# Kernel tuning notes

Hardware: AMD Instinct MI355X
Metric: run time of the kernel (lower is better)

## Reference

```python
import jax, jax.numpy as jnp
import numpy as np


def setup_inputs() -> dict:
    key = jax.random.key(0)
    ks = jax.random.split(key, 14)
    n, c, m, s = 32, 256, 32, 64
    rn = lambda k, shape, sc=1.0: jax.random.normal(k, shape, dtype=jnp.float32) * sc
    return {
        "seg_ori": rn(ks[0], (n, c, m, m)),
        "edge_ori": rn(ks[1], (n, c, m, m)),
        "W_s1": rn(ks[2], (s, c), 0.05), "b_s1": rn(ks[3], (s,), 0.05),
        "W_s11": rn(ks[4], (s, c), 0.05), "b_s11": rn(ks[5], (s,), 0.05),
        "W_mlp": rn(ks[6], (s, c), 0.05), "b_mlp": rn(ks[7], (s,), 0.05),
        "w_s2": rn(ks[8], ()), "b_s2": rn(ks[9], ()),
        "w_s3": rn(ks[10], ()), "b_s3": rn(ks[11], ()),
        "W_g": rn(ks[12], (c, c), 0.02), "b_g": rn(ks[13], (c,), 0.02),
    }


def reference(seg_ori, edge_ori, W_s1, b_s1, W_s11, b_s11, W_mlp, b_mlp,
              w_s2, b_s2, w_s3, b_s3, W_g, b_g):
    n, c, m, _ = seg_ori.shape
    hw = m * m                      # num_n = mids^2
    s = W_s1.shape[0]               # num_s = plane_mid
    seg = seg_ori

    # ---- channel affinity branch ----
    seg_s = jnp.einsum('nchw,sc->nshw', seg, W_s1) + b_s1[None, :, None, None]
    theta_T = seg_s.reshape(n, s, hw)        # view(n, num_s, -1)
    theta = seg_s.reshape(n, hw, s)          # view(n, -1, num_s): reshape, NOT transpose
    ch_att = jax.nn.relu(jnp.mean(seg, axis=(2, 3)) @ W_mlp.T + b_mlp)   # (n, s)
    diag_c = ch_att[:, :, None] * ch_att[:, None, :]                     # (n, s, s) outer
    sim_c = jnp.einsum('nps,nst->npt', theta, diag_c)                    # (n, hw, s)
    sim_c = jax.nn.softmax(jnp.einsum('npt,ntq->npq', sim_c, theta_T), axis=1)  # (n, hw, hw)

    # ---- spatial affinity branch ----
    seg_c = jnp.einsum('nchw,sc->nshw', seg, W_s11) + b_s11[None, :, None, None]
    sigma = seg_c.reshape(n, s, hw)
    sigma_T = seg_c.reshape(n, hw, s)
    sigma_out = jnp.einsum('nps,nsq->npq', sigma_T, sigma)               # (n, hw, hw)
    edge_m = seg * edge_ori
    maxpool_s = jnp.max(seg, axis=1)                                     # (n, m, m)
    edge_m_pool = jnp.max(edge_m, axis=1)                                # (n, m, m)
    seg_ss = (maxpool_s * w_s2 + b_s2).reshape(n, 1, hw)                 # 1x1 conv, 1 channel
    edge_mm = (edge_m_pool * w_s3 + b_s3).reshape(n, hw, 1)
    sim_s = jax.nn.softmax(edge_mm * seg_ss * sigma_out, axis=1)         # (n, hw, hw)

    similarity = sim_c + sim_s

    # ---- GCN: bmm + conv1d(k=1) + relu + residual ----
    seg2 = seg.reshape(n, c, hw)
    seg_sim = jnp.einsum('ncp,npq->ncq', seg2, similarity)               # (n, c, hw)
    out = jax.nn.relu(jnp.einsum('ncl,oc->nol', seg_sim, W_g) + b_g[None, :, None])
    gcn_out = (out + seg2).reshape(n, c, m, m)
    return gcn_out + seg_ori
```

## Files before the change

### kernel.cpp

```cpp
#include <hip/hip_runtime.h>

#define N 32
#define C 256
#define HW 1024
#define S 64
#define LOG2E 1.4426950408889634f

typedef _Float16 f16;
typedef _Float16 f16x4 __attribute__((ext_vector_type(4)));
typedef _Float16 f16x8 __attribute__((ext_vector_type(8)));
typedef float f32x4 __attribute__((ext_vector_type(4)));

#define MFMA(a, b, c) __builtin_amdgcn_mfma_f32_16x16x32_f16(a, b, c, 0, 0, 0)
#define EXP2(x) exp2f(x)

__device__ inline f16x8 lds_ld8(const f16* p) {
    return *(const f16x8*)p;
}

__global__ void __launch_bounds__(256) k_pool1(const float* seg, const float* edge,
        f16* segf, float* pms, float* pme, float* mean,
        const float* Ws1, const float* Ws11, const float* Wg, f16* Wf, f16* Wgf) {
    int n = blockIdx.x, cg = blockIdx.y;
    int t = threadIdx.x, w = t >> 6, lane = t & 63;
    int flat = n * 32 + cg;
    if (flat < 256) {
        int i = flat * 256 + t;
        if (i < S * C) { Wf[i] = (f16)Ws1[i]; Wf[S * C + i] = (f16)Ws11[i]; }
        Wgf[i] = (f16)Wg[i];
    }
    int p4 = (lane << 2) + (w << 8);
    size_t base = (size_t)n * C * HW;
    float4 ms = make_float4(-3e38f, -3e38f, -3e38f, -3e38f);
    float4 me = ms;
    __shared__ float psum[4][8];
    for (int ci = 0; ci < 8; ci++) {
        int c = cg * 8 + ci;
        size_t off = base + (size_t)c * HW + p4;
        float4 s = *(const float4*)(seg + off);
        float4 e = *(const float4*)(edge + off);
        union { f16 h[4]; unsigned long long u; } pk;
        pk.h[0] = (f16)s.x; pk.h[1] = (f16)s.y; pk.h[2] = (f16)s.z; pk.h[3] = (f16)s.w;
        *(unsigned long long*)(segf + off) = pk.u;
        ms.x = fmaxf(ms.x, s.x); ms.y = fmaxf(ms.y, s.y);
        ms.z = fmaxf(ms.z, s.z); ms.w = fmaxf(ms.w, s.w);
        me.x = fmaxf(me.x, s.x * e.x); me.y = fmaxf(me.y, s.y * e.y);
        me.z = fmaxf(me.z, s.z * e.z); me.w = fmaxf(me.w, s.w * e.w);
        float sm = s.x + s.y + s.z + s.w;
        for (int o = 32; o; o >>= 1) sm += __shfl_down(sm, o);
        if (lane == 0) psum[w][ci] = sm;
    }
    __syncthreads();
    if (t < 8)
        mean[n * C + cg * 8 + t] =
            (psum[0][t] + psum[1][t] + psum[2][t] + psum[3][t]) * (1.0f / HW);
    size_t pb = ((size_t)n * 32 + cg) * HW + p4;
    *(float4*)(pms + pb) = ms;
    *(float4*)(pme + pb) = me;
}

__global__ void __launch_bounds__(256) k_pool2(const float* pms, const float* pme,
        float* a2, float* bq, const float* ws2, const float* bs2,
        const float* ws3, const float* bs3,
        const float* mean, const float* Wmlp, const float* bmlp, float* chat) {
    int n = blockIdx.x, t = threadIdx.x;
    int p4 = t << 2;
    float4 ms = make_float4(-3e38f, -3e38f, -3e38f, -3e38f);
    float4 me = ms;
    for (int cg = 0; cg < 32; cg++) {
        size_t pb = ((size_t)n * 32 + cg) * HW + p4;
        float4 a = *(const float4*)(pms + pb);
        float4 b = *(const float4*)(pme + pb);
        ms.x = fmaxf(ms.x, a.x); ms.y = fmaxf(ms.y, a.y);
        ms.z = fmaxf(ms.z, a.z); ms.w = fmaxf(ms.w, a.w);
        me.x = fmaxf(me.x, b.x); me.y = fmaxf(me.y, b.y);
        me.z = fmaxf(me.z, b.z); me.w = fmaxf(me.w, b.w);
    }
    float w3 = ws3[0], b3 = bs3[0], w2 = ws2[0], b2 = bs2[0];
    float4 av, bv;
    av.x = (me.x * w3 + b3) * LOG2E; av.y = (me.y * w3 + b3) * LOG2E;
    av.z = (me.z * w3 + b3) * LOG2E; av.w = (me.w * w3 + b3) * LOG2E;
    bv.x = ms.x * w2 + b2; bv.y = ms.y * w2 + b2;
    bv.z = ms.z * w2 + b2; bv.w = ms.w * w2 + b2;
    *(float4*)(a2 + (size_t)n * HW + p4) = av;
    *(float4*)(bq + (size_t)n * HW + p4) = bv;
    if (t < S) {
        float acc = 0.f;
        const float* wr = Wmlp + (size_t)t * C;
        for (int c = 0; c < C; c++) acc += mean[n * C + c] * wr[c];
        chat[n * S + t] = fmaxf(acc + bmlp[t], 0.f);
    }
}

__global__ void __launch_bounds__(512) k_proj(const f16* segf, const f16* Wf,
        const float* bs1, const float* bs11, const float* chat,
        f16* segc, float* dp2, float* e_, float* dpmm2) {
    int n = blockIdx.x, qt = blockIdx.y;
    int q0 = qt * 64;
    __shared__ f16 sT[64][264];
    __shared__ f16 pT[64][72];
    __shared__ float cA[S];
    const f16* sb = segf + (size_t)n * C * HW + q0;
    int tid = threadIdx.x;
    if (tid < S) cA[tid] = chat[n * S + tid];
    for (int idx = tid; idx < 2048; idx += 512) {
        int c = idx >> 3, q8 = (idx & 7) << 3;
        f16x8 v = *(const f16x8*)(sb + (size_t)c * HW + q8);
        for (int j = 0; j < 8; j++) sT[q8 + j][c] = v[j];
    }
    __syncthreads();
    int lane = tid & 63, wv = tid >> 6;
    int lm = lane & 15, lg = lane >> 4;
    f32x4 acc[4] = {};
    for (int ck = 0; ck < 8; ck++) {
        int c0 = ck * 32;
        f16x8 a0 = *(const f16x8*)(Wf + (size_t)(wv * 16 + lm) * C + c0 + lg * 8);
        for (int j = 0; j < 4; j++) {
            f16x8 b = lds_ld8(&sT[j * 16 + lm][c0 + lg * 8]);
            acc[j] = MFMA(a0, b, acc[j]);
        }
    }
    for (int rr = 0; rr < 4; rr++) {
        int row = wv * 16 + lg * 4 + rr;
        float bias = (row < S) ? bs1[row] : bs11[row - S];
        for (int j = 0; j < 4; j++) {
            int q = q0 + j * 16 + lm;
            float v = acc[j][rr] + bias;
            if (row < S) pT[row][j * 16 + lm] = (f16)v;
            else         segc[((size_t)n * S + (row - S)) * HW + q] = (f16)v;
        }
    }
    __syncthreads();
    if (tid < 64) {
        float a2c = 0.f;
        for (int t = 0; t < S; t += 8) {
            f16x8 v = lds_ld8(&pT[tid][t]);
            for (int j = 0; j < 8; j++) a2c += (float)v[j] * cA[t + j];
        }
        float d2 = a2c * LOG2E;
        dp2[(size_t)n * HW + 16 * tid + qt] = d2;
        float mx = d2, mn = d2;
        for (int o = 32; o; o >>= 1) {
            mx = fmaxf(mx, __shfl_down(mx, o));
            mn = fminf(mn, __shfl_down(mn, o));
        }
        if (tid == 0) {
            dpmm2[(n * 16 + qt) * 2]     = mx;
            dpmm2[(n * 16 + qt) * 2 + 1] = mn;
        }
    } else if (tid < 128) {
        int ql = tid - 64;
        float a2c = 0.f;
        for (int t = 0; t < S; t++) a2c += cA[t] * (float)pT[t][ql];
        e_[(size_t)n * HW + q0 + ql] = a2c;
    }
}

__global__ void __launch_bounds__(512, 4) k_fused(const f16* segf, const f16* segc,
        const float* dp2, const float* e_, const float* a2, const float* bq,
        const float* dpmm2, const f16* Wgf, const float* bg, float* out) {
    int n = blockIdx.x, q0 = blockIdx.y * 64;
    __shared__ f16 bT[64][72];
    __shared__ f16 wT[2][64][136];
    __shared__ float2 da[HW];
    __shared__ float mred[64][9], lred[64][9];
    __shared__ float msL[64], izsL[64], mcL[64], izcL[64];
    const f16* cb = segc + (size_t)n * S * HW;
    const f16* sb = segf + (size_t)n * C * HW;
    int tid = threadIdx.x;
    for (int idx = tid; idx < 64 * 32; idx += 512) {
        int q = idx & 63, th = (idx >> 6) << 1;
        union { f16 h[2]; unsigned u; } pk;
        pk.h[0] = cb[(size_t)th * HW + q0 + q];
        pk.h[1] = cb[(size_t)(th + 1) * HW + q0 + q];
        *(unsigned*)&bT[q][th] = pk.u;
    }
    for (int i = tid; i < HW; i += 512)
        da[i] = make_float2(dp2[(size_t)n * HW + i], a2[(size_t)n * HW + i]);
    __syncthreads();
    int w = tid >> 6, lane = tid & 63, lm = lane & 15, lg = lane >> 4;
    float ev[4], bqv[4];
    for (int j = 0; j < 4; j++) {
        size_t gq = (size_t)n * HW + q0 + j * 16 + lm;
        ev[j] = e_[gq];  bqv[j] = bq[gq];
    }
    float sm[4], sl[4];
    #pragma unroll
    for (int j = 0; j < 4; j++) { sm[j] = -3e38f; sl[j] = 0.f; }
    for (int chk = 0; chk < 8; chk++) {
        int p0 = chk * 128;
        const f16* sp = cb + (size_t)(p0 + w * 16 + lm) * S;
        f16x8 sa0 = *(const f16x8*)(sp + lg * 8);
        f16x8 sa1 = *(const f16x8*)(sp + 32 + lg * 8);
        float avr[4];
        #pragma unroll
        for (int rr = 0; rr < 4; rr++) avr[rr] = da[p0 + w * 16 + lg * 4 + rr].y;
        #pragma unroll
        for (int j = 0; j < 4; j++) {
            f16x8 bb0 = lds_ld8(&bT[j * 16 + lm][lg * 8]);
            f16x8 bb1 = lds_ld8(&bT[j * 16 + lm][32 + lg * 8]);
            f32x4 sg = {};
            sg = MFMA(sa0, bb0, sg);
            sg = MFMA(sa1, bb1, sg);
            float sc[4], fm = -3e38f;
            #pragma unroll
            for (int rr = 0; rr < 4; rr++) {
                sc[rr] = avr[rr] * bqv[j] * sg[rr];
                fm = fmaxf(fm, sc[rr]);
            }
            fm = fmaxf(fm, __shfl_xor(fm, 16));
            fm = fmaxf(fm, __shfl_xor(fm, 32));
            float fl = 0.f;
            #pragma unroll
            for (int rr = 0; rr < 4; rr++) fl += EXP2(sc[rr] - fm);
            fl += __shfl_xor(fl, 16);
            fl += __shfl_xor(fl, 32);
            float nm = fmaxf(sm[j], fm);
            sl[j] = sl[j] * EXP2(sm[j] - nm) + fl * EXP2(fm - nm);
            sm[j] = nm;
        }
    }
    if (lg == 0)
        #pragma unroll
        for (int j = 0; j < 4; j++) {
            mred[j * 16 + lm][w] = sm[j];
            lred[j * 16 + lm][w] = sl[j];
        }
    {
        float mx = -3e38f, mn = 3e38f;
        for (int j2 = 0; j2 < 16; j2++) {
            mx = fmaxf(mx, dpmm2[(n * 16 + j2) * 2]);
            mn = fminf(mn, dpmm2[(n * 16 + j2) * 2 + 1]);
        }
        int qz = tid >> 3, pi = tid & 7;
        float eqz = e_[(size_t)n * HW + q0 + qz];
        float mzv = (eqz > 0.f) ? eqz * mx : eqz * mn;
        float z = 0.f;
        for (int j2 = 0; j2 < 128; j2++) z += EXP2(da[pi + 8 * j2].x * eqz - mzv);
        z += __shfl_xor(z, 1);
        z += __shfl_xor(z, 2);
        z += __shfl_xor(z, 4);
        if (pi == 0) { mcL[qz] = mzv; izcL[qz] = 1.f / z; }
    }
    __syncthreads();
    if (tid < 64) {
        float M = mred[tid][0];
        for (int ww = 1; ww < 8; ww++) M = fmaxf(M, mred[tid][ww]);
        float L = 0.f;
        for (int ww = 0; ww < 8; ww++) L += lred[tid][ww] * EXP2(mred[tid][ww] - M);
        msL[tid] = M; izsL[tid] = 1.f / L;
    }
    __syncthreads();
    float mcv[4], izcv[4], msv[4], izsv[4];
    #pragma unroll
    for (int j = 0; j < 4; j++) {
        int q = j * 16 + lm;
        mcv[j] = mcL[q]; izcv[j] = izcL[q];
        msv[j] = msL[q]; izsv[j] = izsL[q];
    }
    f32x4 acc[2][4] = {};
    for (int chk = 0; chk <= 8; chk++) {
        if (chk > 0) {
            int p0 = (chk - 1) * 128;
            int cur = (chk - 1) & 1;
            #pragma unroll
            for (int ks = 0; ks < 4; ks++) {
                f16x8 a2f[2];
                #pragma unroll
                for (int cf = 0; cf < 2; cf++) {
                    int crow = w * 32 + cf * 16 + lm;
                    a2f[cf] = *(const f16x8*)(sb + (size_t)crow * HW + p0 + ks * 32 + lg * 8);
                }
                #pragma unroll
                for (int qf = 0; qf < 4; qf++) {
                    f16x8 bb = lds_ld8(&wT[cur][qf * 16 + lm][ks * 32 + lg * 8]);
                    acc[0][qf] = MFMA(a2f[0], bb, acc[0][qf]);
                    acc[1][qf] = MFMA(a2f[1], bb, acc[1][qf]);
                }
            }
        }
        if (chk < 8) {
            int p0 = chk * 128;
            const f16* sp = cb + (size_t)(p0 + w * 16 + lm) * S;
            f16x8 sa0 = *(const f16x8*)(sp + lg * 8);
            f16x8 sa1 = *(const f16x8*)(sp + 32 + lg * 8);
            float d2r[4], avr[4];
            #pragma unroll
            for (int rr = 0; rr < 4; rr++) {
                float2 dv = da[p0 + w * 16 + lg * 4 + rr];
                d2r[rr] = dv.x; avr[rr] = dv.y;
            }
            #pragma unroll
            for (int j = 0; j < 4; j++) {
                f16x8 bb0 = lds_ld8(&bT[j * 16 + lm][lg * 8]);
                f16x8 bb1 = lds_ld8(&bT[j * 16 + lm][32 + lg * 8]);
                f32x4 sg = {};
                sg = MFMA(sa0, bb0, sg);
                sg = MFMA(sa1, bb1, sg);
                float wgt[4];
                #pragma unroll
                for (int rr = 0; rr < 4; rr++) {
                    float wc  = EXP2(d2r[rr] * ev[j] - mcv[j]) * izcv[j];
                    float wsv = EXP2(avr[rr] * bqv[j] * sg[rr] - msv[j]) * izsv[j];
                    wgt[rr] = wc + wsv;
                }
                int ql = j * 16 + lm;
                int pp = w * 16 + lg * 4;
                union { f16 h[2]; unsigned u; } c0u, c1u;
                c0u.h[0] = (f16)wgt[0]; c0u.h[1] = (f16)wgt[1];
                c1u.h[0] = (f16)wgt[2]; c1u.h[1] = (f16)wgt[3];
                *(unsigned*)&wT[chk & 1][ql][pp]     = c0u.u;
                *(unsigned*)&wT[chk & 1][ql][pp + 2] = c1u.u;
            }
        }
        __syncthreads();
    }
    f16 (*sT2)[264] = (f16(*)[264])&wT[0][0][0];
    for (int cf = 0; cf < 2; cf++)
        for (int qf = 0; qf < 4; qf++) {
            int crow = w * 32 + cf * 16 + lg * 4;
            int ql = qf * 16 + lm;
            f16x4 pk;
            pk[0] = (f16)acc[cf][qf][0]; pk[1] = (f16)acc[cf][qf][1];
            pk[2] = (f16)acc[cf][qf][2]; pk[3] = (f16)acc[cf][qf][3];
            *(f16x4*)&sT2[ql][crow] = pk;
        }
    __syncthreads();
    int ow = w * 32;
    f32x4 acc2[2][4] = {};
    for (int ck = 0; ck < 8; ck++) {
        int c0 = ck * 32;
        f16x8 af0 = *(const f16x8*)(Wgf + (size_t)(ow + lm) * C + c0 + lg * 8);
        f16x8 af1 = *(const f16x8*)(Wgf + (size_t)(ow + 16 + lm) * C + c0 + lg * 8);
        for (int qf = 0; qf < 4; qf++) {
            f16x8 bf = lds_ld8(&sT2[qf * 16 + lm][c0 + lg * 8]);
            acc2[0][qf] = MFMA(af0, bf, acc2[0][qf]);
            acc2[1][qf] = MFMA(af1, bf, acc2[1][qf]);
        }
    }
    for (int of = 0; of < 2; of++)
        for (int rr = 0; rr < 4; rr++) {
            int o = ow + of * 16 + lg * 4 + rr;
            float bgv = bg[o];
            for (int qf = 0; qf < 4; qf++) {
                int q = q0 + qf * 16 + lm;
                size_t ix = ((size_t)n * C + o) * HW + q;
                out[ix] = fmaxf(acc2[of][qf][rr] + bgv, 0.f) + 2.f * (float)sb[((size_t)o * HW) + q];
            }
        }
}

extern "C" void kernel_launch(void* const* d_in, const int* in_sizes, int n_in,
                              void* d_out, int out_size, void* d_ws, size_t ws_size,
                              hipStream_t stream) {
    const float* seg  = (const float*)d_in[0];
    const float* edge = (const float*)d_in[1];
    const float* Ws1  = (const float*)d_in[2];
    const float* bs1  = (const float*)d_in[3];
    const float* Ws11 = (const float*)d_in[4];
    const float* bs11 = (const float*)d_in[5];
    const float* Wmlp = (const float*)d_in[6];
    const float* bmlp = (const float*)d_in[7];
    const float* ws2  = (const float*)d_in[8];
    const float* bs2  = (const float*)d_in[9];
    const float* ws3  = (const float*)d_in[10];
    const float* bs3  = (const float*)d_in[11];
    const float* Wg   = (const float*)d_in[12];
    const float* bg   = (const float*)d_in[13];
    float* out = (float*)d_out;
    char* wsb = (char*)d_ws;

    f16*   segf   = (f16*)(wsb);
    f16*   segc   = (f16*)(wsb + 16777216);
    float* dpmm2  = (float*)(wsb + 20971520);
    float* pms    = (float*)(wsb + 25165824);
    float* pme    = (float*)(wsb + 29360128);
    f16*   Wf     = (f16*)(wsb + 41943040);
    f16*   Wgf    = (f16*)(wsb + 42008576);
    float* mean   = (float*)(wsb + 42139648);
    float* chat   = (float*)(wsb + 42172416);
    float* dp2    = (float*)(wsb + 42180608);
    float* e_     = (float*)(wsb + 42311680);
    float* a2     = (float*)(wsb + 42442752);
    float* bq     = (float*)(wsb + 42573824);

    k_pool1<<<dim3(32, 32), 256, 0, stream>>>(seg, edge, segf, pms, pme, mean,
                                              Ws1, Ws11, Wg, Wf, Wgf);
    k_pool2<<<32, 256, 0, stream>>>(pms, pme, a2, bq, ws2, bs2, ws3, bs3,
                                    mean, Wmlp, bmlp, chat);
    k_proj<<<dim3(32, 16), 512, 0, stream>>>(segf, Wf, bs1, bs11, chat,
                                             segc, dp2, e_, dpmm2);
    k_fused<<<dim3(32, 16), 512, 0, stream>>>(segf, segc, dp2, e_, a2, bq,
                                              dpmm2, Wgf, bg, out);
}
```

Before: 228.9 us.

## Fuse two pooling kernels into one and compute channel MLP inside projection

Merges the two pooling kernels into a single kernel. Each block covers 128 pixels across all 256 channels, so the channel max finishes in shared memory. The per-channel mean is accumulated with atomics into a buffer zeroed by a memset, and the channel-attention MLP is recomputed inside each projection block. This removes one launch and the intermediate partial-max buffers' round trip through global memory. The cost is a smaller grid with lower occupancy during the bandwidth-bound read, a large LDS tile, and a mean computed from fp16-rounded values.

```diff
diff --git a/kernel.cpp b/kernel.cpp
--- a/kernel.cpp
+++ b/kernel.cpp
@@ -18,97 +18,89 @@
     return *(const f16x8*)p;
 }
 
-__global__ void __launch_bounds__(256) k_pool1(const float* seg, const float* edge,
-        f16* segf, float* pms, float* pme, float* mean,
+__global__ void __launch_bounds__(256) k_pool(const float* seg, const float* edge,
+        f16* segf, float* a2, float* bq, float* mean,
+        const float* ws2, const float* bs2, const float* ws3, const float* bs3,
         const float* Ws1, const float* Ws11, const float* Wg, f16* Wf, f16* Wgf) {
-    int n = blockIdx.x, cg = blockIdx.y;
-    int t = threadIdx.x, w = t >> 6, lane = t & 63;
-    int flat = n * 32 + cg;
-    if (flat < 256) {
-        int i = flat * 256 + t;
+    int n = blockIdx.x, hg = blockIdx.y;
+    int t = threadIdx.x;
+    {
+        int i = (n * 8 + hg) * 256 + t;
         if (i < S * C) { Wf[i] = (f16)Ws1[i]; Wf[S * C + i] = (f16)Ws11[i]; }
         Wgf[i] = (f16)Wg[i];
     }
-    int p4 = (lane << 2) + (w << 8);
-    size_t base = (size_t)n * C * HW;
+    __shared__ f16 sT16[256][132];
+    __shared__ float psS[8][128], psE[8][128];
+    int hl = (t & 31) << 2;
+    int cg = t >> 5;
+    size_t base = (size_t)n * C * HW + hg * 128 + hl;
     float4 ms = make_float4(-3e38f, -3e38f, -3e38f, -3e38f);
     float4 me = ms;
-    __shared__ float psum[4][8];
-    for (int ci = 0; ci < 8; ci++) {
-        int c = cg * 8 + ci;
-        size_t off = base + (size_t)c * HW + p4;
+    for (int ci = 0; ci < 32; ci++) {
+        int c = cg * 32 + ci;
+        size_t off = base + (size_t)c * HW;
         float4 s = *(const float4*)(seg + off);
         float4 e = *(const float4*)(edge + off);
         union { f16 h[4]; unsigned long long u; } pk;
         pk.h[0] = (f16)s.x; pk.h[1] = (f16)s.y; pk.h[2] = (f16)s.z; pk.h[3] = (f16)s.w;
         *(unsigned long long*)(segf + off) = pk.u;
+        *(unsigned long long*)&sT16[c][hl] = pk.u;
         ms.x = fmaxf(ms.x, s.x); ms.y = fmaxf(ms.y, s.y);
         ms.z = fmaxf(ms.z, s.z); ms.w = fmaxf(ms.w, s.w);
         me.x = fmaxf(me.x, s.x * e.x); me.y = fmaxf(me.y, s.y * e.y);
         me.z = fmaxf(me.z, s.z * e.z); me.w = fmaxf(me.w, s.w * e.w);
-        float sm = s.x + s.y + s.z + s.w;
-        for (int o = 32; o; o >>= 1) sm += __shfl_down(sm, o);
-        if (lane == 0) psum[w][ci] = sm;
-    }
-    __syncthreads();
-    if (t < 8)
-        mean[n * C + cg * 8 + t] =
-            (psum[0][t] + psum[1][t] + psum[2][t] + psum[3][t]) * (1.0f / HW);
-    size_t pb = ((size_t)n * 32 + cg) * HW + p4;
-    *(float4*)(pms + pb) = ms;
-    *(float4*)(pme + pb) = me;
-}
-
-__global__ void __launch_bounds__(256) k_pool2(const float* pms, const float* pme,
-        float* a2, float* bq, const float* ws2, const float* bs2,
-        const float* ws3, const float* bs3,
-        const float* mean, const float* Wmlp, const float* bmlp, float* chat) {
-    int n = blockIdx.x, t = threadIdx.x;
-    int p4 = t << 2;
-    float4 ms = make_float4(-3e38f, -3e38f, -3e38f, -3e38f);
-    float4 me = ms;
-    for (int cg = 0; cg < 32; cg++) {
-        size_t pb = ((size_t)n * 32 + cg) * HW + p4;
-        float4 a = *(const float4*)(pms + pb);
-        float4 b = *(const float4*)(pme + pb);
-        ms.x = fmaxf(ms.x, a.x); ms.y = fmaxf(ms.y, a.y);
-        ms.z = fmaxf(ms.z, a.z); ms.w = fmaxf(ms.w, a.w);
-        me.x = fmaxf(me.x, b.x); me.y = fmaxf(me.y, b.y);
-        me.z = fmaxf(me.z, b.z); me.w = fmaxf(me.w, b.w);
-    }
-    float w3 = ws3[0], b3 = bs3[0], w2 = ws2[0], b2 = bs2[0];
-    float4 av, bv;
-    av.x = (me.x * w3 + b3) * LOG2E; av.y = (me.y * w3 + b3) * LOG2E;
-    av.z = (me.z * w3 + b3) * LOG2E; av.w = (me.w * w3 + b3) * LOG2E;
-    bv.x = ms.x * w2 + b2; bv.y = ms.y * w2 + b2;
-    bv.z = ms.z * w2 + b2; bv.w = ms.w * w2 + b2;
-    *(float4*)(a2 + (size_t)n * HW + p4) = av;
-    *(float4*)(bq + (size_t)n * HW + p4) = bv;
-    if (t < S) {
-        float acc = 0.f;
-        const float* wr = Wmlp + (size_t)t * C;
-        for (int c = 0; c < C; c++) acc += mean[n * C + c] * wr[c];
-        chat[n * S + t] = fmaxf(acc + bmlp[t], 0.f);
+    }
+    *(float4*)&psS[cg][hl] = ms;
+    *(float4*)&psE[cg][hl] = me;
+    __syncthreads();
+    float sm = 0.f;
+    for (int j = 0; j < 128; j += 4) {
+        f16x4 v = *(const f16x4*)&sT16[t][j];
+        sm += (float)v[0] + (float)v[1] + (float)v[2] + (float)v[3];
+    }
+    atomicAdd(&mean[n * C + t], sm * (1.0f / HW));
+    if (t < 128) {
+        float M = -3e38f, E = -3e38f;
+        for (int g = 0; g < 8; g++) {
+            M = fmaxf(M, psS[g][t]);
+            E = fmaxf(E, psE[g][t]);
+        }
+        float w3 = ws3[0], b3 = bs3[0], w2 = ws2[0], b2 = bs2[0];
+        size_t gq = (size_t)n * HW + hg * 128 + t;
+        a2[gq] = (E * w3 + b3) * LOG2E;
+        bq[gq] = M * w2 + b2;
     }
 }
 
 __global__ void __launch_bounds__(512) k_proj(const f16* segf, const f16* Wf,
-        const float* bs1, const float* bs11, const float* chat,
+        const float* bs1, const float* bs11, const float* mean,
+        const float* Wmlp, const float* bmlp,
         f16* segc, float* dp2, float* e_, float* dpmm2) {
     int n = blockIdx.x, qt = blockIdx.y;
     int q0 = qt * 64;
     __shared__ f16 sT[64][264];
     __shared__ f16 pT[64][72];
     __shared__ float cA[S];
+    __shared__ float cpart[S][4];
     const f16* sb = segf + (size_t)n * C * HW + q0;
     int tid = threadIdx.x;
-    if (tid < S) cA[tid] = chat[n * S + tid];
     for (int idx = tid; idx < 2048; idx += 512) {
         int c = idx >> 3, q8 = (idx & 7) << 3;
         f16x8 v = *(const f16x8*)(sb + (size_t)c * HW + q8);
         for (int j = 0; j < 8; j++) sT[q8 + j][c] = v[j];
     }
-    __syncthreads();
+    if (tid < 256) {
+        int s = tid >> 2, qp = tid & 3;
+        const float* wr = Wmlp + (size_t)s * C + qp * 64;
+        const float* mr = mean + (size_t)n * C + qp * 64;
+        float acc = 0.f;
+        for (int i = 0; i < 64; i++) acc += mr[i] * wr[i];
+        cpart[s][qp] = acc;
+    }
+    __syncthreads();
+    if (tid < S)
+        cA[tid] = fmaxf(cpart[tid][0] + cpart[tid][1] + cpart[tid][2]
+                        + cpart[tid][3] + bmlp[tid], 0.f);
     int lane = tid & 63, wv = tid >> 6;
     int lm = lane & 15, lg = lane >> 4;
     f32x4 acc[4] = {};
@@ -373,23 +365,20 @@
     f16*   segf   = (f16*)(wsb);
     f16*   segc   = (f16*)(wsb + 16777216);
     float* dpmm2  = (float*)(wsb + 20971520);
-    float* pms    = (float*)(wsb + 25165824);
-    float* pme    = (float*)(wsb + 29360128);
     f16*   Wf     = (f16*)(wsb + 41943040);
     f16*   Wgf    = (f16*)(wsb + 42008576);
     float* mean   = (float*)(wsb + 42139648);
-    float* chat   = (float*)(wsb + 42172416);
     float* dp2    = (float*)(wsb + 42180608);
     float* e_     = (float*)(wsb + 42311680);
     float* a2     = (float*)(wsb + 42442752);
     float* bq     = (float*)(wsb + 42573824);
 
-    k_pool1<<<dim3(32, 32), 256, 0, stream>>>(seg, edge, segf, pms, pme, mean,
-                                              Ws1, Ws11, Wg, Wf, Wgf);
-    k_pool2<<<32, 256, 0, stream>>>(pms, pme, a2, bq, ws2, bs2, ws3, bs3,
-                                    mean, Wmlp, bmlp, chat);
-    k_proj<<<dim3(32, 16), 512, 0, stream>>>(segf, Wf, bs1, bs11, chat,
-                                             segc, dp2, e_, dpmm2);
+    hipMemsetAsync(mean, 0, N * C * sizeof(float), stream);
+    k_pool<<<dim3(32, 8), 256, 0, stream>>>(seg, edge, segf, a2, bq, mean,
+                                            ws2, bs2, ws3, bs3,
+                                            Ws1, Ws11, Wg, Wf, Wgf);
+    k_proj<<<dim3(32, 16), 512, 0, stream>>>(segf, Wf, bs1, bs11, mean,
+                                             Wmlp, bmlp, segc, dp2, e_, dpmm2);
     k_fused<<<dim3(32, 16), 512, 0, stream>>>(segf, segc, dp2, e_, a2, bq,
                                               dpmm2, Wgf, bg, out);
 }
```

Result: slower. 237.1 us (+3.6%).
